# Performance work log

Measured on AMD Instinct MI355X. Metric: run time of the kernel, lower is better.

The kernel has to match this reference:

```python
import jax, jax.numpy as jnp
import numpy as np

NUM_HEADS = 8
NUM_GROUPS = 32
EPS = 1e-5
RESCALE = 1.0


def setup_inputs() -> dict:
    key = jax.random.key(0)
    ks = jax.random.split(key, 7)
    b, c, h, w = 16, 512, 32, 32
    return {
        "x": jax.random.normal(ks[0], (b, c, h, w), jnp.float32),
        "norm_w": jax.random.normal(ks[1], (c,), jnp.float32),
        "norm_b": jax.random.normal(ks[2], (c,), jnp.float32),
        "qkv_w": jax.random.normal(ks[3], (3 * c, c), jnp.float32) * (c ** -0.5),
        "qkv_b": jax.random.normal(ks[4], (3 * c,), jnp.float32) * 0.02,
        "proj_w": jax.random.normal(ks[5], (c, c), jnp.float32) * (c ** -0.5),
        "proj_b": jax.random.normal(ks[6], (c,), jnp.float32) * 0.02,
    }


def _group_norm(x, w, b):
    # x: [B, C, L]
    B, C, L = x.shape
    g = x.reshape(B, NUM_GROUPS, (C // NUM_GROUPS) * L)
    mu = jnp.mean(g, axis=-1, keepdims=True)
    var = jnp.var(g, axis=-1, keepdims=True)
    g = (g - mu) * jax.lax.rsqrt(var + EPS)
    return g.reshape(B, C, L) * w[None, :, None] + b[None, :, None]


def reference(x, norm_w, norm_b, qkv_w, qkv_b, proj_w, proj_b):
    b, c, hh, ww = x.shape
    L = hh * ww
    H = NUM_HEADS
    ch = c // H  # head dim

    xr = x.reshape(b, c, L)
    hid = _group_norm(xr, norm_w, norm_b)

    # 1x1 conv1d == matmul over channel dim: [3c, c] @ [b, c, L]
    qkv = jnp.einsum('oc,bcl->bol', qkv_w, hid) + qkv_b[None, :, None]
    # torch: reshape(b*H, 3*ch, L).split(ch) -> per-head contiguous [q|k|v] blocks
    qkv = qkv.reshape(b, H, 3, ch, L)
    q, k, v = qkv[:, :, 0], qkv[:, :, 1], qkv[:, :, 2]  # [b, H, ch, L]

    scale = 1.0 / (ch ** 0.25)
    weight = jnp.einsum('bhct,bhcs->bhts', q * scale, k * scale)
    weight = jax.nn.softmax(weight.astype(jnp.float32), axis=-1).astype(weight.dtype)
    a = jnp.einsum('bhts,bhcs->bhct', weight, v)  # [b, H, ch, L]

    h = a.reshape(b, c, L)
    h = jnp.einsum('oc,bcl->bol', proj_w, h) + proj_b[None, :, None]
    h = h.reshape(b, c, hh, ww)
    return (x + h) / RESCALE
```

## Files before the change

### kernel.cpp

```cpp
#include <hip/hip_runtime.h>
#include <hip/hip_bf16.h>
#include <stdint.h>


using f32x4  = __attribute__((ext_vector_type(4))) float;
using bf16x8 = __attribute__((ext_vector_type(8))) __bf16;
using s8v    = __attribute__((ext_vector_type(8))) short;
using s4v    = __attribute__((ext_vector_type(4))) short;

__device__ __forceinline__ short f2bf(float f){
  union { float f; unsigned u; } c; c.f = f;
  unsigned r = (c.u + 0x7FFFu + ((c.u >> 16) & 1u)) >> 16;
  return (short)r;
}

__device__ __forceinline__ float exp2_fast(float x){
#if __has_builtin(__builtin_amdgcn_exp2f)
  return __builtin_amdgcn_exp2f(x);
#else
  return exp2f(x);
#endif
}

__device__ __forceinline__ void gl_lds16(const void* g, void* l){
  __builtin_amdgcn_global_load_lds((const __attribute__((address_space(1))) void*)g,
                                   (__attribute__((address_space(3))) void*)l, 16, 0, 0);
}

__global__ void k_convw(const float* __restrict__ qw, const float* __restrict__ pw,
                        const float* __restrict__ qb,
                        short* __restrict__ qwb, short* __restrict__ pwb,
                        float* __restrict__ qbp){
  int i = blockIdx.x * 256 + threadIdx.x;
  if (i < 786432){
    int o = i >> 9, kk = i & 511;
    int h = o / 192, rem = o - h*192;
    int nr = (rem >> 6)*512 + h*64 + (rem & 63);
    qwb[nr*512 + kk] = f2bf(qw[i]);
  } else if (i < 1048576){
    int j = i - 786432;
    pwb[j] = f2bf(pw[j]);
  } else if (i < 1050112){
    int o = i - 1048576;
    int h = o / 192, rem = o - h*192;
    qbp[(rem >> 6)*512 + h*64 + (rem & 63)] = qb[o];
  }
}

__global__ __launch_bounds__(256) void k_gnorm(const float* __restrict__ x,
                                               const float* __restrict__ w,
                                               const float* __restrict__ bia,
                                               short* __restrict__ hid){
  int b = blockIdx.x >> 5;
  int g = blockIdx.x & 31;
  int tid = threadIdx.x;
  const float* xg = x + ((size_t)b*512 + g*16)*1024;
  int l0 = tid * 4;
  float v[16][4];
  float s1 = 0.f, s2 = 0.f;
  #pragma unroll
  for (int c = 0; c < 16; c++){
    f32x4 t = *(const f32x4*)(xg + c*1024 + l0);
    #pragma unroll
    for (int j = 0; j < 4; j++){ v[c][j] = t[j]; s1 += t[j]; s2 += t[j]*t[j]; }
  }
  #pragma unroll
  for (int m = 32; m; m >>= 1){ s1 += __shfl_xor(s1, m); s2 += __shfl_xor(s2, m); }
  __shared__ float r1[4], r2[4];
  int wv = tid >> 6, ln = tid & 63;
  if (ln == 0){ r1[wv] = s1; r2[wv] = s2; }
  __syncthreads();
  s1 = r1[0]+r1[1]+r1[2]+r1[3];
  s2 = r2[0]+r2[1]+r2[2]+r2[3];
  float mu = s1 * (1.f/16384.f);
  float var = s2 * (1.f/16384.f) - mu*mu;
  float rs = rsqrtf(var + 1e-5f);
  float ww[16], bb[16];
  #pragma unroll
  for (int c = 0; c < 16; c++){ ww[c] = w[g*16+c]*rs; bb[c] = bia[g*16+c]; }
  #pragma unroll
  for (int j = 0; j < 4; j++){
    short o[16];
    #pragma unroll
    for (int c = 0; c < 16; c++) o[c] = f2bf((v[c][j]-mu)*ww[c] + bb[c]);
    short* dst = hid + ((size_t)(b*1024 + l0 + j))*512 + g*16;
    *(s8v*)dst     = *(s8v*)o;
    *(s8v*)(dst+8) = *(s8v*)(o+8);
  }
}

template<int EPI>
__global__ __launch_bounds__(256) void k_gemm(
    const short* __restrict__ A, const short* __restrict__ Bm,
    const float* __restrict__ bias, const float* __restrict__ xres,
    short* __restrict__ q_t, short* __restrict__ k_t, short* __restrict__ v_t,
    float* __restrict__ outp)
{
  __shared__ short Lds[16384];
  int id = blockIdx.x;
  int xcd = id & 7, ix = id >> 3;
  int mt, nt;
  if (EPI == 0){ mt = ix % 12; nt = ix / 12; }
  else         { mt = ix & 3;  nt = ix >> 2; }
  int m0 = mt * 128;
  int n0 = (xcd + 8*nt) * 128;
  int tid = threadIdx.x;
  int lane = tid & 63;
  int wv = tid >> 6;
  int wr = wv >> 1, wc = wv & 1;
  int l15 = lane & 15, g = lane >> 4;
  f32x4 acc[4][4] = {};

  auto STAGE = [&](int db, int t){
    int k0 = t * 32;
    #pragma unroll
    for (int i = 0; i < 4; i++){
      int cc = wv*4 + i;
      int c2 = cc & 7;
      int row = c2*16 + (lane>>2), slot = lane & 3;
      const short* src = (cc < 8 ? A + (size_t)(m0+row)*512
                                 : Bm + (size_t)(n0+row)*512)
                         + k0 + ((slot ^ ((row>>1)&3))*8);
      char* dst = (char*)Lds + db*16384 + (cc < 8 ? 0 : 8192) + c2*1024;
      gl_lds16(src, dst);
    }
  };

  auto COMPUTE = [&](int db){
    const char* Ab = (const char*)Lds + db*16384;
    const char* Bb = Ab + 8192;
    bf16x8 af[4], bf[4];
    #pragma unroll
    for (int m = 0; m < 4; m++){
      int row = wr*64 + m*16 + l15;
      af[m] = *(const bf16x8*)(Ab + row*64 + ((g*16) ^ (((row>>1)&3)<<4)));
    }
    #pragma unroll
    for (int n = 0; n < 4; n++){
      int row = wc*64 + n*16 + l15;
      bf[n] = *(const bf16x8*)(Bb + row*64 + ((g*16) ^ (((row>>1)&3)<<4)));
    }
    __builtin_amdgcn_s_setprio(1);
    #pragma unroll
    for (int m = 0; m < 4; m++)
      #pragma unroll
      for (int n = 0; n < 4; n++)
        acc[m][n] = __builtin_amdgcn_mfma_f32_16x16x32_bf16(af[m], bf[n], acc[m][n], 0, 0, 0);
    __builtin_amdgcn_s_setprio(0);
  };

  STAGE(0, 0);
  for (int t = 0; t < 16; t++){
    asm volatile("s_waitcnt vmcnt(0)" ::: "memory");
    __builtin_amdgcn_s_barrier();
    if (t < 15) STAGE((t+1)&1, t+1);
    COMPUTE(t&1);
  }
  __builtin_amdgcn_s_barrier();

  if (EPI == 0){
    int sel = m0 >> 9;
    if (sel < 2){
      const float sc = (sel == 0) ? 0.18033688011112042f : 1.0f;
      short* dstb = (sel == 0) ? q_t : k_t;
      #pragma unroll
      for (int m = 0; m < 4; m++){
        int ob = m0 + wr*64 + m*16 + (g<<2);
        int hh = (ob>>6)&7, c0 = ob&63;
        float bs[4];
        #pragma unroll
        for (int r = 0; r < 4; r++) bs[r] = bias[ob+r];
        #pragma unroll
        for (int n = 0; n < 4; n++){
          int nn = n0 + wc*64 + n*16 + l15;
          int bb = nn >> 10, ll = nn & 1023;
          int bh = bb*8 + hh;
          short o4[4];
          #pragma unroll
          for (int r = 0; r < 4; r++) o4[r] = f2bf((acc[m][n][r] + bs[r]) * sc);
          *(s4v*)(dstb + ((size_t)bh*1024 + ll)*64 + c0) = *(s4v*)o4;
        }
      }
    } else {
      short* Sc = Lds;
      #pragma unroll
      for (int m = 0; m < 4; m++){
        int ob = m0 + wr*64 + m*16 + (g<<2);
        int h2 = (ob>>6)&1, cq = (ob>>4)&3;
        float bs[4];
        #pragma unroll
        for (int r = 0; r < 4; r++) bs[r] = bias[ob+r];
        #pragma unroll
        for (int n = 0; n < 4; n++){
          int nn = n0 + wc*64 + n*16 + l15;
          int sl = nn & 63, sreg = (nn>>6)&1;
          int ks2 = sl >> 5, gq = (sl>>2)&3, i2 = (sl&3) + 4*((sl>>4)&1);
          int base = (h2*2 + sreg)*4096 + (((ks2*4+gq)*4 + cq)*16 + (g<<2))*8 + i2;
          #pragma unroll
          for (int r = 0; r < 4; r++)
            Sc[base + r*8] = f2bf(acc[m][n][r] + bs[r]);
        }
      }
      __syncthreads();
      int b0  = n0 >> 10;
      int s64 = (n0 >> 6) & 15;
      int hb  = (m0 - 1024) >> 6;
      #pragma unroll
      for (int it = 0; it < 8; it++){
        int flat = it*2048 + tid*8;
        int h2 = flat >> 13, rem = flat & 8191, sreg = rem >> 12, off = rem & 4095;
        int bh = b0*8 + hb + h2;
        *(s8v*)(v_t + ((size_t)bh*16 + s64 + sreg)*4096 + off) = *(const s8v*)(Sc + flat);
      }
    }
  } else {
    #pragma unroll
    for (int m = 0; m < 4; m++){
      int ob = m0 + wr*64 + m*16 + (g<<2);
      float bs[4];
      #pragma unroll
      for (int r = 0; r < 4; r++) bs[r] = bias[ob+r];
      #pragma unroll
      for (int n = 0; n < 4; n++){
        int nn = n0 + wc*64 + n*16 + l15;
        int bb = nn >> 10, ll = nn & 1023;
        #pragma unroll
        for (int r = 0; r < 4; r++){
          size_t idx = ((size_t)bb*512 + ob + r)*1024 + ll;
          outp[idx] = xres[idx] + acc[m][n][r] + bs[r];
        }
      }
    }
  }
}

__global__ __launch_bounds__(256, 4) void k_attn(
    const short* __restrict__ q_t, const short* __restrict__ k_t,
    const short* __restrict__ v_t, short* __restrict__ a_bt)
{
  __shared__ short Kh[4*2048];
  __shared__ short Vh[4*2048];
  int id = blockIdx.x;
  int xcd = id & 7, ix = id >> 3;
  int bh = xcd*16 + (ix >> 3);
  int qb = ix & 7;
  int bb = bh >> 3, hh = bh & 7;
  int tid = threadIdx.x;
  int lane = tid & 63;
  int wv = tid >> 6;
  int l15 = lane & 15, g = lane >> 4;

  bf16x8 qf[2][2];
  #pragma unroll
  for (int qt = 0; qt < 2; qt++){
    const short* qbase = q_t + ((size_t)bh*1024 + qb*128 + qt*64 + wv*16 + l15)*64 + g*8;
    qf[qt][0] = *(const bf16x8*)(qbase);
    qf[qt][1] = *(const bf16x8*)(qbase + 32);
  }
  asm volatile("" :: "v"(qf[0][0]), "v"(qf[0][1]), "v"(qf[1][0]), "v"(qf[1][1]));

  bf16x8 onesb;
  #pragma unroll
  for (int i = 0; i < 8; i++) onesb[i] = (__bf16)1.0f;

  f32x4 o[2][4] = {};
  f32x4 osum[2] = {};

  auto STAGE = [&](int db, int h){
    int t64 = h >> 1, ks = h & 1;
    #pragma unroll
    for (int i = 0; i < 2; i++){
      int cc = wv*2 + i;
      if (cc < 4){
        int row = cc*8 + (lane>>3), slot = lane & 7;
        gl_lds16(k_t + ((size_t)bh*1024 + h*32 + row)*64 + ((slot ^ (row&7))*8),
                 (char*)Kh + db*4096 + cc*1024);
      } else {
        gl_lds16(v_t + ((size_t)bh*16 + t64)*4096 + ks*2048 + (cc-4)*512 + lane*8,
                 (char*)Vh + db*4096 + (cc-4)*1024);
      }
    }
  };

  auto COMPUTE = [&](int db){
    const char* Kb = (const char*)Kh + db*4096;
    const char* Vb = (const char*)Vh + db*4096;
    f32x4 scl[2][2] = {};
    #pragma unroll
    for (int jl = 0; jl < 2; jl++){
      int row = jl*16 + l15;
      int swz = (row&7)<<4;
      bf16x8 kf0 = *(const bf16x8*)(Kb + row*128 + ((g*16) ^ swz));
      bf16x8 kf1 = *(const bf16x8*)(Kb + row*128 + ((64 + g*16) ^ swz));
      __builtin_amdgcn_s_setprio(1);
      #pragma unroll
      for (int qt = 0; qt < 2; qt++){
        scl[qt][jl] = __builtin_amdgcn_mfma_f32_16x16x32_bf16(kf0, qf[qt][0], scl[qt][jl], 0, 0, 0);
        scl[qt][jl] = __builtin_amdgcn_mfma_f32_16x16x32_bf16(kf1, qf[qt][1], scl[qt][jl], 0, 0, 0);
      }
      __builtin_amdgcn_s_setprio(0);
    }
    bf16x8 pa[2];
    #pragma unroll
    for (int qt = 0; qt < 2; qt++){
      #pragma unroll
      for (int i2 = 0; i2 < 8; i2++)
        pa[qt][i2] = (__bf16)exp2_fast(scl[qt][i2>>2][i2&3]);
      osum[qt] = __builtin_amdgcn_mfma_f32_16x16x32_bf16(pa[qt], onesb, osum[qt], 0, 0, 0);
    }
    #pragma unroll
    for (int jd = 0; jd < 4; jd++){
      bf16x8 vbb = *(const bf16x8*)(Vb + (g*4+jd)*256 + l15*16);
      __builtin_amdgcn_s_setprio(1);
      #pragma unroll
      for (int qt = 0; qt < 2; qt++)
        o[qt][jd] = __builtin_amdgcn_mfma_f32_16x16x32_bf16(pa[qt], vbb, o[qt][jd], 0, 0, 0);
      __builtin_amdgcn_s_setprio(0);
    }
  };

  STAGE(0, 0);
  STAGE(1, 1);
  #pragma unroll 2
  for (int h = 0; h < 30; h++){
    STAGE((h+2)&3, h+2);
    asm volatile("s_waitcnt vmcnt(4)" ::: "memory");
    __builtin_amdgcn_s_barrier();
    COMPUTE(h&3);
  }
  asm volatile("s_waitcnt vmcnt(2)" ::: "memory");
  __builtin_amdgcn_s_barrier();
  COMPUTE(2);
  asm volatile("s_waitcnt vmcnt(0)" ::: "memory");
  __builtin_amdgcn_s_barrier();
  COMPUTE(3);

  #pragma unroll
  for (int qt = 0; qt < 2; qt++){
    #pragma unroll
    for (int r = 0; r < 4; r++){
      float inv = 1.f / osum[qt][r];
      int qrow = qb*128 + qt*64 + wv*16 + g*4 + r;
      #pragma unroll
      for (int jd = 0; jd < 4; jd++)
        a_bt[((size_t)bb*1024 + qrow)*512 + hh*64 + jd*16 + l15] = f2bf(o[qt][jd][r] * inv);
    }
  }
}

extern "C" void kernel_launch(void* const* d_in, const int* in_sizes, int n_in,
                              void* d_out, int out_size, void* d_ws, size_t ws_size,
                              hipStream_t stream){
  const float* x  = (const float*)d_in[0];
  const float* nw = (const float*)d_in[1];
  const float* nb = (const float*)d_in[2];
  const float* qw = (const float*)d_in[3];
  const float* qb = (const float*)d_in[4];
  const float* pw = (const float*)d_in[5];
  const float* pb = (const float*)d_in[6];
  float* outp = (float*)d_out;

  char* ws = (char*)d_ws;
  short* hid  = (short*)(ws);
  short* qwb  = (short*)(ws + 16777216);
  short* pwb  = (short*)(ws + 18350080);
  short* q_t  = (short*)(ws + 18874368);
  short* k_t  = (short*)(ws + 35651584);
  short* v_t  = (short*)(ws + 52428800);
  short* a_bt = hid;
  float* qbp  = (float*)d_out;
  if (ws_size < 69206016) return;

  k_convw<<<4103, 256, 0, stream>>>(qw, pw, qb, qwb, pwb, qbp);
  k_gnorm<<<512, 256, 0, stream>>>(x, nw, nb, hid);
  k_gemm<0><<<1536, 256, 0, stream>>>(qwb, hid, qbp, nullptr, q_t, k_t, v_t, nullptr);
  k_attn<<<1024, 256, 0, stream>>>(q_t, k_t, v_t, a_bt);
  k_gemm<1><<<512, 256, 0, stream>>>(pwb, a_bt, pb, x, nullptr, nullptr, nullptr, outp);
}
```

Baseline: 129.2 us.

## Merge weight conversion into groupnorm kernel and deepen GEMM K-tile to 64

```diff
diff --git a/kernel.cpp b/kernel.cpp
--- a/kernel.cpp
+++ b/kernel.cpp
@@ -27,33 +27,37 @@
                                    (__attribute__((address_space(3))) void*)l, 16, 0, 0);
 }
 
-__global__ void k_convw(const float* __restrict__ qw, const float* __restrict__ pw,
-                        const float* __restrict__ qb,
-                        short* __restrict__ qwb, short* __restrict__ pwb,
-                        float* __restrict__ qbp){
-  int i = blockIdx.x * 256 + threadIdx.x;
-  if (i < 786432){
-    int o = i >> 9, kk = i & 511;
-    int h = o / 192, rem = o - h*192;
-    int nr = (rem >> 6)*512 + h*64 + (rem & 63);
-    qwb[nr*512 + kk] = f2bf(qw[i]);
-  } else if (i < 1048576){
-    int j = i - 786432;
-    pwb[j] = f2bf(pw[j]);
-  } else if (i < 1050112){
-    int o = i - 1048576;
-    int h = o / 192, rem = o - h*192;
-    qbp[(rem >> 6)*512 + h*64 + (rem & 63)] = qb[o];
-  }
-}
-
-__global__ __launch_bounds__(256) void k_gnorm(const float* __restrict__ x,
-                                               const float* __restrict__ w,
-                                               const float* __restrict__ bia,
-                                               short* __restrict__ hid){
-  int b = blockIdx.x >> 5;
-  int g = blockIdx.x & 31;
+__global__ __launch_bounds__(256) void k_pre(const float* __restrict__ x,
+                                             const float* __restrict__ w,
+                                             const float* __restrict__ bia,
+                                             short* __restrict__ hid,
+                                             const float* __restrict__ qw,
+                                             const float* __restrict__ pw,
+                                             const float* __restrict__ qb,
+                                             short* __restrict__ qwb,
+                                             short* __restrict__ pwb,
+                                             float* __restrict__ qbp){
+  int bid = blockIdx.x;
   int tid = threadIdx.x;
+  if (bid >= 512){
+    int i = (bid - 512) * 256 + tid;
+    if (i < 786432){
+      int o = i >> 9, kk = i & 511;
+      int h = o / 192, rem = o - h*192;
+      int nr = (rem >> 6)*512 + h*64 + (rem & 63);
+      qwb[nr*512 + kk] = f2bf(qw[i]);
+    } else if (i < 1048576){
+      int j = i - 786432;
+      pwb[j] = f2bf(pw[j]);
+    } else if (i < 1050112){
+      int o = i - 1048576;
+      int h = o / 192, rem = o - h*192;
+      qbp[(rem >> 6)*512 + h*64 + (rem & 63)] = qb[o];
+    }
+    return;
+  }
+  int b = bid >> 5;
+  int g = bid & 31;
   const float* xg = x + ((size_t)b*512 + g*16)*1024;
   int l0 = tid * 4;
   float v[16][4];
@@ -96,7 +100,8 @@
     short* __restrict__ q_t, short* __restrict__ k_t, short* __restrict__ v_t,
     float* __restrict__ outp)
 {
-  __shared__ short Lds[16384];
+  __shared__ short Al[2][128*64];
+  __shared__ short Bl[2][128*64];
   int id = blockIdx.x;
   int xcd = id & 7, ix = id >> 3;
   int mt, nt;
@@ -112,51 +117,57 @@
   f32x4 acc[4][4] = {};
 
   auto STAGE = [&](int db, int t){
-    int k0 = t * 32;
-    #pragma unroll
-    for (int i = 0; i < 4; i++){
-      int cc = wv*4 + i;
-      int c2 = cc & 7;
-      int row = c2*16 + (lane>>2), slot = lane & 3;
-      const short* src = (cc < 8 ? A + (size_t)(m0+row)*512
-                                 : Bm + (size_t)(n0+row)*512)
-                         + k0 + ((slot ^ ((row>>1)&3))*8);
-      char* dst = (char*)Lds + db*16384 + (cc < 8 ? 0 : 8192) + c2*1024;
-      gl_lds16(src, dst);
+    int k0 = t * 64;
+    #pragma unroll
+    for (int i = 0; i < 8; i++){
+      int cc = wv*8 + i;
+      if (cc < 16){
+        int slot = cc*64 + lane;
+        int row = slot >> 3, off = slot & 7;
+        gl_lds16(A + (size_t)(m0+row)*512 + k0 + (off ^ (row&7))*8,
+                 (char*)Al[db] + cc*1024);
+      } else {
+        int slot = (cc-16)*64 + lane;
+        int row = slot >> 3, off = slot & 7;
+        gl_lds16(Bm + (size_t)(n0+row)*512 + k0 + (off ^ (row&7))*8,
+                 (char*)Bl[db] + (cc-16)*1024);
+      }
     }
   };
 
   auto COMPUTE = [&](int db){
-    const char* Ab = (const char*)Lds + db*16384;
-    const char* Bb = Ab + 8192;
-    bf16x8 af[4], bf[4];
-    #pragma unroll
-    for (int m = 0; m < 4; m++){
-      int row = wr*64 + m*16 + l15;
-      af[m] = *(const bf16x8*)(Ab + row*64 + ((g*16) ^ (((row>>1)&3)<<4)));
-    }
-    #pragma unroll
-    for (int n = 0; n < 4; n++){
-      int row = wc*64 + n*16 + l15;
-      bf[n] = *(const bf16x8*)(Bb + row*64 + ((g*16) ^ (((row>>1)&3)<<4)));
-    }
-    __builtin_amdgcn_s_setprio(1);
-    #pragma unroll
-    for (int m = 0; m < 4; m++)
-      #pragma unroll
-      for (int n = 0; n < 4; n++)
-        acc[m][n] = __builtin_amdgcn_mfma_f32_16x16x32_bf16(af[m], bf[n], acc[m][n], 0, 0, 0);
-    __builtin_amdgcn_s_setprio(0);
+    #pragma unroll
+    for (int kk = 0; kk < 2; kk++){
+      bf16x8 af[4], bf[4];
+      #pragma unroll
+      for (int m = 0; m < 4; m++){
+        int row = wr*64 + m*16 + l15;
+        int byte = row*128 + (((kk*64) + (g*16)) ^ ((row&7)<<4));
+        af[m] = *(const bf16x8*)((char*)Al[db] + byte);
+      }
+      #pragma unroll
+      for (int n = 0; n < 4; n++){
+        int row = wc*64 + n*16 + l15;
+        int byte = row*128 + (((kk*64) + (g*16)) ^ ((row&7)<<4));
+        bf[n] = *(const bf16x8*)((char*)Bl[db] + byte);
+      }
+      __builtin_amdgcn_s_setprio(1);
+      #pragma unroll
+      for (int m = 0; m < 4; m++)
+        #pragma unroll
+        for (int n = 0; n < 4; n++)
+          acc[m][n] = __builtin_amdgcn_mfma_f32_16x16x32_bf16(af[m], bf[n], acc[m][n], 0, 0, 0);
+      __builtin_amdgcn_s_setprio(0);
+    }
   };
 
   STAGE(0, 0);
-  for (int t = 0; t < 16; t++){
-    asm volatile("s_waitcnt vmcnt(0)" ::: "memory");
-    __builtin_amdgcn_s_barrier();
-    if (t < 15) STAGE((t+1)&1, t+1);
+  for (int t = 0; t < 8; t++){
+    __syncthreads();
+    if (t < 7) STAGE((t+1)&1, t+1);
     COMPUTE(t&1);
   }
-  __builtin_amdgcn_s_barrier();
+  __syncthreads();
 
   if (EPI == 0){
     int sel = m0 >> 9;
@@ -182,7 +193,7 @@
         }
       }
     } else {
-      short* Sc = Lds;
+      short* Sc = (short*)Al;
       #pragma unroll
       for (int m = 0; m < 4; m++){
         int ob = m0 + wr*64 + m*16 + (g<<2);
@@ -326,13 +337,16 @@
     STAGE((h+2)&3, h+2);
     asm volatile("s_waitcnt vmcnt(4)" ::: "memory");
     __builtin_amdgcn_s_barrier();
+    __builtin_amdgcn_sched_barrier(0);
     COMPUTE(h&3);
   }
   asm volatile("s_waitcnt vmcnt(2)" ::: "memory");
   __builtin_amdgcn_s_barrier();
+  __builtin_amdgcn_sched_barrier(0);
   COMPUTE(2);
   asm volatile("s_waitcnt vmcnt(0)" ::: "memory");
   __builtin_amdgcn_s_barrier();
+  __builtin_amdgcn_sched_barrier(0);
   COMPUTE(3);
 
   #pragma unroll
@@ -371,8 +385,7 @@
   float* qbp  = (float*)d_out;
   if (ws_size < 69206016) return;
 
-  k_convw<<<4103, 256, 0, stream>>>(qw, pw, qb, qwb, pwb, qbp);
-  k_gnorm<<<512, 256, 0, stream>>>(x, nw, nb, hid);
+  k_pre<<<4615, 256, 0, stream>>>(x, nw, nb, hid, qw, pw, qb, qwb, pwb, qbp);
   k_gemm<0><<<1536, 256, 0, stream>>>(qwb, hid, qbp, nullptr, q_t, k_t, v_t, nullptr);
   k_attn<<<1024, 256, 0, stream>>>(q_t, k_t, v_t, a_bt);
   k_gemm<1><<<512, 256, 0, stream>>>(pwb, a_bt, pb, x, nullptr, nullptr, nullptr, outp);
```

Result: faster. 119.5 us (-7.5%).
